# Kernel tuning notes

Hardware: AMD Instinct MI355X
Metric: run time of the kernel (lower is better)

The kernel has to match this reference:

```python
import jax, jax.numpy as jnp
import numpy as np

FS = 30.0        # sampling rate
N = 512          # input_size (time samples)
BIN_RES = 0.001  # frequency resolution
C, S = 32, 256   # channel / spatial dims of x
F_LO, F_HI = 0.66, 2.5


def _chirp_consts():
    """Deterministic CZT constants, matching the torch module's construction."""
    freq_zoom = np.arange(F_LO, F_HI, BIN_RES, dtype=np.float64)
    M = len(freq_zoom)  # 1840
    dt = 1.0 / FS  # (t[-1]-t[0])/(N-1) == 1/fs for t = arange(N)/fs
    df = (freq_zoom[-1] - freq_zoom[0]) / (M - 1)
    # A (phase ramp) diagonal values: 2*pi*f0*(-k)*dt, k = 0..N-1
    k = np.arange(N)
    a_vals = 2.0 * np.pi * freq_zoom[0] * (-k) * dt
    a_cos = np.cos(a_vals).astype(np.float32)
    a_sin = np.sin(a_vals).astype(np.float32)
    # W chirp matrix: -2*pi*df*k*n*dt, k in [0,M), n in [0,N)
    kv = np.arange(M)[:, None]
    nv = np.arange(N)[None, :]
    w_vals = -2.0 * np.pi * df * kv * nv * dt
    W_real = np.cos(w_vals).astype(np.float32)
    W_imag = np.sin(w_vals).astype(np.float32)
    return W_real, W_imag, a_cos, a_sin


def setup_inputs() -> dict:
    key = jax.random.key(0)
    x = jax.random.normal(key, (N, C, S), dtype=jnp.float32)
    W_real, W_imag, a_cos, a_sin = _chirp_consts()
    return {
        "x": x,
        "W_real": jnp.asarray(W_real),
        "W_imag": jnp.asarray(W_imag),
        "a_cos": jnp.asarray(a_cos),
        "a_sin": jnp.asarray(a_sin),
    }


def reference(x, W_real, W_imag, a_cos, a_sin):
    # A is diagonal -> diag matmul == per-row broadcast scaling (same math).
    Ax_real = a_cos[:, None, None] * x  # [N, C, S]
    Ax_imag = a_sin[:, None, None] * x  # [N, C, S]
    Ax = jnp.concatenate([Ax_real, Ax_imag], axis=0)  # [2N, C, S]
    # Block chirp matrix [[Wr, -Wi], [Wi, Wr]] -> [2M, 2N]
    W = jnp.concatenate(
        [
            jnp.concatenate([W_real, -W_imag], axis=1),
            jnp.concatenate([W_imag, W_real], axis=1),
        ],
        axis=0,
    )
    W = jnp.clip(W, -1.0, 1.0)  # Hardtanh (no-op on cos/sin, kept for fidelity)
    X = jnp.einsum("ji,ics->jcs", W, Ax)  # [2M, C, S]
    return W, X
```

## Files before the change

kernel.cpp:

```cpp
#include <hip/hip_runtime.h>
#include <hip/hip_bf16.h>
#include <stdint.h>

#define MM   1840
#define M2   3680
#define NN   512
#define K2   1024
#define CS   8192
#define MPAD 3712

typedef __bf16 bf16x8 __attribute__((ext_vector_type(8)));
typedef float  floatx4 __attribute__((ext_vector_type(4)));

__global__ __launch_bounds__(256) void czt_wout(const float* __restrict__ Wr,
                                                const float* __restrict__ Wi,
                                                float* __restrict__ Wout) {
    const int j  = blockIdx.x;
    const int c4 = threadIdx.x * 4;
    const int jj = (j < MM) ? j : j - MM;
    const bool top = (j < MM);
    const bool first = (c4 < NN);
    const int col = first ? c4 : c4 - NN;

    float4 v;
    if (top) {
        if (first) {
            v = *(const float4*)&Wr[(size_t)jj * NN + col];
        } else {
            v = *(const float4*)&Wi[(size_t)jj * NN + col];
            v.x = -v.x; v.y = -v.y; v.z = -v.z; v.w = -v.w;
        }
    } else {
        if (first) v = *(const float4*)&Wi[(size_t)jj * NN + col];
        else       v = *(const float4*)&Wr[(size_t)jj * NN + col];
    }
    v.x = fminf(1.0f, fmaxf(-1.0f, v.x));
    v.y = fminf(1.0f, fmaxf(-1.0f, v.y));
    v.z = fminf(1.0f, fmaxf(-1.0f, v.z));
    v.w = fminf(1.0f, fmaxf(-1.0f, v.w));
    *(float4*)&Wout[(size_t)j * K2 + c4] = v;
}

__global__ __launch_bounds__(128) void czt_aprep(const float* __restrict__ Wr,
                                                 const float* __restrict__ Wi,
                                                 const float* __restrict__ ac,
                                                 const float* __restrict__ as_,
                                                 __hip_bfloat16* __restrict__ Abf) {
    const int j = blockIdx.x;
    const int k = threadIdx.x * 4;

    union { __hip_bfloat16 h[4]; uint2 u; } p;
    if (j < M2) {
        const int jj = (j < MM) ? j : j - MM;
        const float4 wr = *(const float4*)&Wr[(size_t)jj * NN + k];
        const float4 wi = *(const float4*)&Wi[(size_t)jj * NN + k];
        const float4 c  = *(const float4*)&ac[k];
        const float4 s  = *(const float4*)&as_[k];
        float v0, v1, v2, v3;
        if (j < MM) {
            v0 = wr.x * c.x - wi.x * s.x;
            v1 = wr.y * c.y - wi.y * s.y;
            v2 = wr.z * c.z - wi.z * s.z;
            v3 = wr.w * c.w - wi.w * s.w;
        } else {
            v0 = wi.x * c.x + wr.x * s.x;
            v1 = wi.y * c.y + wr.y * s.y;
            v2 = wi.z * c.z + wr.z * s.z;
            v3 = wi.w * c.w + wr.w * s.w;
        }
        p.h[0] = __float2bfloat16(v0);
        p.h[1] = __float2bfloat16(v1);
        p.h[2] = __float2bfloat16(v2);
        p.h[3] = __float2bfloat16(v3);
    } else {
        p.h[0] = __float2bfloat16(0.0f);
        p.h[1] = __float2bfloat16(0.0f);
        p.h[2] = __float2bfloat16(0.0f);
        p.h[3] = __float2bfloat16(0.0f);
    }
    *(uint2*)&Abf[(size_t)j * NN + k] = p.u;
}

__global__ __launch_bounds__(256) void czt_xt(const float* __restrict__ x,
                                              __hip_bfloat16* __restrict__ Bxt) {
    __shared__ float tile[32][33];
    const int tx = threadIdx.x;
    const int ty = threadIdx.y;
    const int n0 = blockIdx.x * 32;
    const int k0 = blockIdx.y * 32;

#pragma unroll
    for (int i = 0; i < 4; ++i) {
        const int k = k0 + ty + i * 8;
        tile[ty + i * 8][tx] = x[(size_t)k * CS + n0 + tx];
    }
    __syncthreads();
#pragma unroll
    for (int i = 0; i < 4; ++i) {
        const int n = n0 + ty + i * 8;
        Bxt[(size_t)n * NN + k0 + tx] = __float2bfloat16(tile[tx][ty + i * 8]);
    }
}

__device__ __forceinline__ void gload_lds16(const void* g, void* l) {
    __builtin_amdgcn_global_load_lds(
        (const __attribute__((address_space(1))) uint32_t*)g,
        (__attribute__((address_space(3))) uint32_t*)l,
        16, 0, 0);
}

__global__ __launch_bounds__(256) void czt_gemm(const __hip_bfloat16* __restrict__ Abf,
                                                const __hip_bfloat16* __restrict__ Bxt,
                                                float* __restrict__ Xout) {
    __shared__ __hip_bfloat16 As[128 * 64];
    __shared__ __hip_bfloat16 Bs[128 * 64];

    const int tid  = threadIdx.x;
    const int lane = tid & 63;
    const int w    = tid >> 6;
    const int quad = lane >> 4;
    const int r16  = lane & 15;

    const int mtile = blockIdx.y * 128;
    const int ntile = blockIdx.x * 128;
    const int wm = (w >> 1) * 64;
    const int wn = (w & 1) * 64;

    const int rstage = w * 32 + (lane >> 3);
    const int cstage = (lane & 7) * 8;
    const __hip_bfloat16* Ag = Abf + (size_t)(mtile + rstage) * NN + cstage;
    const __hip_bfloat16* Bg = Bxt + (size_t)(ntile + rstage) * NN + cstage;

    floatx4 acc[4][4] = {};

#pragma unroll 1
    for (int kt = 0; kt < NN / 64; ++kt) {
        __syncthreads();
#pragma unroll
        for (int t = 0; t < 4; ++t) {
            gload_lds16(Ag + (size_t)(t * 8) * NN + kt * 64, &As[(w * 32 + t * 8) * 64]);
            gload_lds16(Bg + (size_t)(t * 8) * NN + kt * 64, &Bs[(w * 32 + t * 8) * 64]);
        }
        __syncthreads();

#pragma unroll
        for (int ks = 0; ks < 2; ++ks) {
            bf16x8 af[4], bfr[4];
#pragma unroll
            for (int i = 0; i < 4; ++i) {
                af[i]  = *(const bf16x8*)&As[(wm + i * 16 + r16) * 64 + ks * 32 + quad * 8];
                bfr[i] = *(const bf16x8*)&Bs[(wn + i * 16 + r16) * 64 + ks * 32 + quad * 8];
            }
#pragma unroll
            for (int i = 0; i < 4; ++i)
#pragma unroll
                for (int jn = 0; jn < 4; ++jn)
                    acc[i][jn] = __builtin_amdgcn_mfma_f32_16x16x32_bf16(
                        af[i], bfr[jn], acc[i][jn], 0, 0, 0);
        }
    }

#pragma unroll
    for (int i = 0; i < 4; ++i) {
        const int rbase = mtile + wm + i * 16 + quad * 4;
#pragma unroll
        for (int rr = 0; rr < 4; ++rr) {
            const int rg = rbase + rr;
            if (rg < M2) {
#pragma unroll
                for (int jn = 0; jn < 4; ++jn) {
                    const int cg = ntile + wn + jn * 16 + r16;
                    Xout[(size_t)rg * CS + cg] = acc[i][jn][rr];
                }
            }
        }
    }
}

extern "C" void kernel_launch(void* const* d_in, const int* in_sizes, int n_in,
                              void* d_out, int out_size, void* d_ws, size_t ws_size,
                              hipStream_t stream) {
    const float* x   = (const float*)d_in[0];
    const float* Wr  = (const float*)d_in[1];
    const float* Wi  = (const float*)d_in[2];
    const float* ac  = (const float*)d_in[3];
    const float* as_ = (const float*)d_in[4];

    float* Wout = (float*)d_out;
    float* Xout = (float*)d_out + (size_t)M2 * K2;

    __hip_bfloat16* Abf = (__hip_bfloat16*)d_ws;
    __hip_bfloat16* Bxt = (__hip_bfloat16*)((char*)d_ws + (size_t)MPAD * NN * 2);

    czt_wout <<<dim3(M2),        dim3(256),     0, stream>>>(Wr, Wi, Wout);
    czt_aprep<<<dim3(MPAD),      dim3(128),     0, stream>>>(Wr, Wi, ac, as_, Abf);
    czt_xt   <<<dim3(CS / 32, NN / 32), dim3(32, 8), 0, stream>>>(x, Bxt);
    czt_gemm <<<dim3(CS / 128, MPAD / 128), dim3(256), 0, stream>>>(Abf, Bxt, Xout);
}
```

Measured before the change: 199.8 us.

## Fuse W output, A prep and x transpose into one prep kernel

Merges the three preprocessing kernels (W block matrix output, phase-folded bf16 A matrix, transposed bf16 x) into a single launch that splits work by block index. Each W row is now read once for both the fp32 W output and the bf16 A operand. The x transpose uses 64x32 tiles with float4 loads and 16-byte bf16 stores. This cuts launch overhead and redundant reads of W, with the GEMM unchanged.

```diff
diff --git a/kernel.cpp b/kernel.cpp
--- a/kernel.cpp
+++ b/kernel.cpp
@@ -9,96 +9,89 @@
 #define CS   8192
 #define MPAD 3712
 
+#define WPREP_BLOCKS (MPAD / 2)
+#define XT_NB        (CS / 32)
+#define XT_KB        (NN / 64)
+
 typedef __bf16 bf16x8 __attribute__((ext_vector_type(8)));
 typedef float  floatx4 __attribute__((ext_vector_type(4)));
 
-__global__ __launch_bounds__(256) void czt_wout(const float* __restrict__ Wr,
+__global__ __launch_bounds__(256) void czt_prep(const float* __restrict__ Wr,
                                                 const float* __restrict__ Wi,
-                                                float* __restrict__ Wout) {
-    const int j  = blockIdx.x;
-    const int c4 = threadIdx.x * 4;
-    const int jj = (j < MM) ? j : j - MM;
-    const bool top = (j < MM);
-    const bool first = (c4 < NN);
-    const int col = first ? c4 : c4 - NN;
+                                                const float* __restrict__ ac,
+                                                const float* __restrict__ as_,
+                                                const float* __restrict__ x,
+                                                float* __restrict__ Wout,
+                                                __hip_bfloat16* __restrict__ Abf,
+                                                __hip_bfloat16* __restrict__ Bxt) {
+    __shared__ float tile[64 * 33];
+    const int b   = blockIdx.x;
+    const int tid = threadIdx.x;
 
-    float4 v;
-    if (top) {
-        if (first) {
-            v = *(const float4*)&Wr[(size_t)jj * NN + col];
+    if (b < WPREP_BLOCKS) {
+        const int j = b * 2 + (tid >> 7);
+        const int k = (tid & 127) * 4;
+
+        union { __hip_bfloat16 h[4]; uint2 u; } p;
+        if (j < M2) {
+            const int jj = (j < MM) ? j : j - MM;
+            const float4 wr = *(const float4*)&Wr[(size_t)jj * NN + k];
+            const float4 wi = *(const float4*)&Wi[(size_t)jj * NN + k];
+            const float4 c  = *(const float4*)&ac[k];
+            const float4 s  = *(const float4*)&as_[k];
+            float4 f, g;
+            float a0, a1, a2, a3;
+            if (j < MM) {
+                f = wr;
+                g.x = -wi.x; g.y = -wi.y; g.z = -wi.z; g.w = -wi.w;
+                a0 = wr.x * c.x - wi.x * s.x;
+                a1 = wr.y * c.y - wi.y * s.y;
+                a2 = wr.z * c.z - wi.z * s.z;
+                a3 = wr.w * c.w - wi.w * s.w;
+            } else {
+                f = wi;
+                g = wr;
+                a0 = wi.x * c.x + wr.x * s.x;
+                a1 = wi.y * c.y + wr.y * s.y;
+                a2 = wi.z * c.z + wr.z * s.z;
+                a3 = wi.w * c.w + wr.w * s.w;
+            }
+            f.x = fminf(1.f, fmaxf(-1.f, f.x)); f.y = fminf(1.f, fmaxf(-1.f, f.y));
+            f.z = fminf(1.f, fmaxf(-1.f, f.z)); f.w = fminf(1.f, fmaxf(-1.f, f.w));
+            g.x = fminf(1.f, fmaxf(-1.f, g.x)); g.y = fminf(1.f, fmaxf(-1.f, g.y));
+            g.z = fminf(1.f, fmaxf(-1.f, g.z)); g.w = fminf(1.f, fmaxf(-1.f, g.w));
+            *(float4*)&Wout[(size_t)j * K2 + k]      = f;
+            *(float4*)&Wout[(size_t)j * K2 + NN + k] = g;
+            p.h[0] = __float2bfloat16(a0);
+            p.h[1] = __float2bfloat16(a1);
+            p.h[2] = __float2bfloat16(a2);
+            p.h[3] = __float2bfloat16(a3);
         } else {
-            v = *(const float4*)&Wi[(size_t)jj * NN + col];
-            v.x = -v.x; v.y = -v.y; v.z = -v.z; v.w = -v.w;
+            p.h[0] = p.h[1] = p.h[2] = p.h[3] = __float2bfloat16(0.0f);
         }
+        *(uint2*)&Abf[(size_t)j * NN + k] = p.u;
     } else {
-        if (first) v = *(const float4*)&Wi[(size_t)jj * NN + col];
-        else       v = *(const float4*)&Wr[(size_t)jj * NN + col];
-    }
-    v.x = fminf(1.0f, fmaxf(-1.0f, v.x));
-    v.y = fminf(1.0f, fmaxf(-1.0f, v.y));
-    v.z = fminf(1.0f, fmaxf(-1.0f, v.z));
-    v.w = fminf(1.0f, fmaxf(-1.0f, v.w));
-    *(float4*)&Wout[(size_t)j * K2 + c4] = v;
-}
+        const int tb = b - WPREP_BLOCKS;
+        const int n0 = (tb & (XT_NB - 1)) * 32;
+        const int k0 = (tb >> 8) * 64;
 
-__global__ __launch_bounds__(128) void czt_aprep(const float* __restrict__ Wr,
-                                                 const float* __restrict__ Wi,
-                                                 const float* __restrict__ ac,
-                                                 const float* __restrict__ as_,
-                                                 __hip_bfloat16* __restrict__ Abf) {
-    const int j = blockIdx.x;
-    const int k = threadIdx.x * 4;
+        const int row = tid >> 2;
+        const int c8  = (tid & 3) * 8;
+        const float* src = &x[(size_t)(k0 + row) * CS + n0 + c8];
+        const float4 v0 = *(const float4*)src;
+        const float4 v1 = *(const float4*)(src + 4);
+        float* tr = &tile[row * 33 + c8];
+        tr[0] = v0.x; tr[1] = v0.y; tr[2] = v0.z; tr[3] = v0.w;
+        tr[4] = v1.x; tr[5] = v1.y; tr[6] = v1.z; tr[7] = v1.w;
+        __syncthreads();
 
-    union { __hip_bfloat16 h[4]; uint2 u; } p;
-    if (j < M2) {
-        const int jj = (j < MM) ? j : j - MM;
-        const float4 wr = *(const float4*)&Wr[(size_t)jj * NN + k];
-        const float4 wi = *(const float4*)&Wi[(size_t)jj * NN + k];
-        const float4 c  = *(const float4*)&ac[k];
-        const float4 s  = *(const float4*)&as_[k];
-        float v0, v1, v2, v3;
-        if (j < MM) {
-            v0 = wr.x * c.x - wi.x * s.x;
-            v1 = wr.y * c.y - wi.y * s.y;
-            v2 = wr.z * c.z - wi.z * s.z;
-            v3 = wr.w * c.w - wi.w * s.w;
-        } else {
-            v0 = wi.x * c.x + wr.x * s.x;
-            v1 = wi.y * c.y + wr.y * s.y;
-            v2 = wi.z * c.z + wr.z * s.z;
-            v3 = wi.w * c.w + wr.w * s.w;
-        }
-        p.h[0] = __float2bfloat16(v0);
-        p.h[1] = __float2bfloat16(v1);
-        p.h[2] = __float2bfloat16(v2);
-        p.h[3] = __float2bfloat16(v3);
-    } else {
-        p.h[0] = __float2bfloat16(0.0f);
-        p.h[1] = __float2bfloat16(0.0f);
-        p.h[2] = __float2bfloat16(0.0f);
-        p.h[3] = __float2bfloat16(0.0f);
-    }
-    *(uint2*)&Abf[(size_t)j * NN + k] = p.u;
-}
-
-__global__ __launch_bounds__(256) void czt_xt(const float* __restrict__ x,
-                                              __hip_bfloat16* __restrict__ Bxt) {
-    __shared__ float tile[32][33];
-    const int tx = threadIdx.x;
-    const int ty = threadIdx.y;
-    const int n0 = blockIdx.x * 32;
-    const int k0 = blockIdx.y * 32;
-
+        const int oc = tid & 7;
+        const int nr = tid >> 3;
+        union { __hip_bfloat16 h[8]; uint4 u; } q;
 #pragma unroll
-    for (int i = 0; i < 4; ++i) {
-        const int k = k0 + ty + i * 8;
-        tile[ty + i * 8][tx] = x[(size_t)k * CS + n0 + tx];
-    }
-    __syncthreads();
-#pragma unroll
-    for (int i = 0; i < 4; ++i) {
-        const int n = n0 + ty + i * 8;
-        Bxt[(size_t)n * NN + k0 + tx] = __float2bfloat16(tile[tx][ty + i * 8]);
+        for (int jj = 0; jj < 8; ++jj)
+            q.h[jj] = __float2bfloat16(tile[(oc * 8 + jj) * 33 + nr]);
+        *(uint4*)&Bxt[(size_t)(n0 + nr) * NN + k0 + oc * 8] = q.u;
     }
 }
 
@@ -192,8 +185,7 @@
     __hip_bfloat16* Abf = (__hip_bfloat16*)d_ws;
     __hip_bfloat16* Bxt = (__hip_bfloat16*)((char*)d_ws + (size_t)MPAD * NN * 2);
 
-    czt_wout <<<dim3(M2),        dim3(256),     0, stream>>>(Wr, Wi, Wout);
-    czt_aprep<<<dim3(MPAD),      dim3(128),     0, stream>>>(Wr, Wi, ac, as_, Abf);
-    czt_xt   <<<dim3(CS / 32, NN / 32), dim3(32, 8), 0, stream>>>(x, Bxt);
-    czt_gemm <<<dim3(CS / 128, MPAD / 128), dim3(256), 0, stream>>>(Abf, Bxt, Xout);
+    czt_prep<<<dim3(WPREP_BLOCKS + XT_NB * XT_KB), dim3(256), 0, stream>>>(
+        Wr, Wi, ac, as_, x, Wout, Abf, Bxt);
+    czt_gemm<<<dim3(CS / 128, MPAD / 128), dim3(256), 0, stream>>>(Abf, Bxt, Xout);
 }
```

Result: faster. 194.7 us (-2.5%).
